# Performance work log

Hardware: AMD Instinct MI355X
Metric: run time of the kernel (lower is better)

## Reference

```python
import jax, jax.numpy as jnp
import numpy as np

N_NODES = 50000
N_EDGES = 800000
NUM_FEATURES = 128
HIDDEN = 128
NUM_CLASSES = 32


def gcn_conv(x, src, dst, n, W, b):
    loop = jnp.arange(n)
    s = jnp.concatenate([src, loop])
    d = jnp.concatenate([dst, loop])
    deg = jax.ops.segment_sum(jnp.ones_like(d, dtype=x.dtype), d, num_segments=n)
    dinv = jnp.where(deg > 0, jax.lax.rsqrt(deg), 0.0)
    norm = dinv[s] * dinv[d]                      # [E+n]
    h = x @ W                                     # [n, out]
    msg = h[s] * norm[:, None]                    # gather + scale
    out = jax.ops.segment_sum(msg, d, num_segments=n)  # scatter-add
    return out + b


def setup_inputs() -> dict:
    key = jax.random.key(0)
    ks = jax.random.split(key, 9)
    x = jax.random.normal(ks[0], (N_NODES, NUM_FEATURES), dtype=jnp.float32)
    edge_index = jax.random.randint(ks[1], (2, N_EDGES), 0, N_NODES, dtype=jnp.int64)
    sc1 = 1.0 / np.sqrt(NUM_FEATURES)
    sc2 = 1.0 / np.sqrt(HIDDEN)
    W1 = jax.random.uniform(ks[2], (NUM_FEATURES, HIDDEN), jnp.float32, -sc1, sc1)
    b1 = jnp.zeros((HIDDEN,), jnp.float32)
    W2 = jax.random.uniform(ks[3], (HIDDEN, HIDDEN), jnp.float32, -sc2, sc2)
    b2 = jnp.zeros((HIDDEN,), jnp.float32)
    Wfc = jax.random.uniform(ks[4], (HIDDEN, NUM_CLASSES), jnp.float32, -sc2, sc2)
    bfc = jax.random.uniform(ks[5], (NUM_CLASSES,), jnp.float32, -sc2, sc2)
    return {"x": x, "edge_index": edge_index, "W1": W1, "b1": b1,
            "W2": W2, "b2": b2, "Wfc": Wfc, "bfc": bfc}


def reference(x, edge_index, W1, b1, W2, b2, Wfc, bfc):
    n = x.shape[0]
    src, dst = edge_index[0], edge_index[1]
    h = jax.nn.relu(gcn_conv(x, src, dst, n, W1, b1))
    h = jax.nn.relu(gcn_conv(h, src, dst, n, W2, b2))
    # global_mean_pool with batch = zeros -> mean over all nodes, shape [1, HIDDEN]
    pooled = jnp.mean(h, axis=0, keepdims=True)
    return pooled @ Wfc + bfc  # [1, NUM_CLASSES]
```

## Files before the change

kernel.cpp:

```cpp
#include <hip/hip_runtime.h>
#include <stdint.h>

#define FEAT 128
#define ECH 2048
#define CAP 200000

typedef short bf16x8 __attribute__((ext_vector_type(8)));
typedef float f32x4 __attribute__((ext_vector_type(4)));
typedef float f32x2 __attribute__((ext_vector_type(2)));

__device__ __forceinline__ float bfs(unsigned short u) {
    uint32_t t = ((uint32_t)u) << 16;
    return __builtin_bit_cast(float, t);
}
__device__ __forceinline__ unsigned short f2bf(float f) {
    uint32_t u = __builtin_bit_cast(uint32_t, f);
    u += 0x7fffu + ((u >> 16) & 1u);
    return (unsigned short)(u >> 16);
}

__launch_bounds__(256)
__global__ void k_prep(const int* __restrict__ ei,
                       int* __restrict__ dstb, int* __restrict__ srcb,
                       int* __restrict__ bcnt, int* __restrict__ deg,
                       int E, int n, int psz, int NE,
                       const void* W1, const void* W2,
                       const void* b1, const void* b2,
                       const void* Wfc, const void* bfc,
                       unsigned short* Wth1, unsigned short* Wth2,
                       float* b1f, float* b2f, float* Wfcf, float* bfcf) {
    int t = threadIdx.x;

    if ((int)blockIdx.x >= NE) {
        __shared__ int hits;
        int blk = blockIdx.x - NE;
        const void* sampsrc = (blk < 32) ? W1 : (blk < 64 ? W2 : Wfc);
        const uint32_t* samp = (const uint32_t*)sampsrc;
        if (t == 0) hits = 0;
        __syncthreads();
        unsigned ew = (samp[t] >> 7) & 0xFFu;
        unsigned long long bl = __ballot(ew >= 0x60u && ew <= 0x90u);
        if ((t & 63) == 0) atomicAdd(&hits, (int)__popcll(bl));
        __syncthreads();
        int isbf = (2 * hits > 256);

        if (blk < 64) {
            const void* W = (blk < 32) ? W1 : W2;
            unsigned short* th = (blk < 32) ? Wth1 : Wth2;
            int base = (blk & 31) * 512;
            #pragma unroll
            for (int j = 0; j < 2; j++) {
                int idx = base + t * 2 + j;
                int nn = idx >> 7, k = idx & 127;
                int si = k * 128 + nn;
                float f = isbf ? bfs(((const unsigned short*)W)[si])
                               : ((const float*)W)[si];
                th[nn * 128 + k] = f2bf(f);
            }
        } else {
            int i = (blk - 64) * 256 + t;
            if (i >= 4384) return;
            const void* src; float* dst; int off;
            if (i < 128)       { src = b1;  dst = b1f;  off = i; }
            else if (i < 256)  { src = b2;  dst = b2f;  off = i - 128; }
            else if (i < 4352) { src = Wfc; dst = Wfcf; off = i - 256; }
            else               { src = bfc; dst = bfcf; off = i - 4352; }
            dst[off] = isbf ? bfs(((const unsigned short*)src)[off])
                            : ((const float*)src)[off];
        }
        return;
    }

    __shared__ int lflag;
    __shared__ int cnt[8], lofs[8], gbase[8];
    __shared__ int stage_s[ECH];
    __shared__ int stage_d[ECH];
    __shared__ char sb[ECH];
    if (t < 128) {
        int di = blockIdx.x * 128 + t;
        if (di < n) deg[di] = 0;
    }
    if (t == 0) lflag = 0;
    if (t < 8) cnt[t] = 0;
    __syncthreads();
    if (ei[1 + 2 * t] != 0) atomicOr(&lflag, 1);
    __syncthreads();
    int is32 = lflag;

    int base = blockIdx.x * ECH;
    int s[8], d[8], p[8], slot[8];
    #pragma unroll
    for (int j = 0; j < 8; j++) {
        int e = base + j * 256 + t;
        int ss = 0, dd = 0;
        if (e < E) {
            ss = is32 ? ei[e]     : ei[2 * e];
            dd = is32 ? ei[E + e] : ei[2 * E + 2 * e];
            if ((unsigned)ss >= (unsigned)n) ss = 0;
            if ((unsigned)dd >= (unsigned)n) dd = 0;
            int pp = dd / psz;
            if (pp > 7) pp = 7;
            p[j] = pp;
            slot[j] = atomicAdd(&cnt[pp], 1);
        } else p[j] = -1;
        s[j] = ss; d[j] = dd;
    }
    __syncthreads();
    if (t == 0) {
        int acc = 0;
        #pragma unroll
        for (int i = 0; i < 8; i++) { lofs[i] = acc; acc += cnt[i]; }
    }
    __syncthreads();
    if (t < 8) gbase[t] = atomicAdd(&bcnt[t], cnt[t]);
    __syncthreads();
    #pragma unroll
    for (int j = 0; j < 8; j++) {
        if (p[j] >= 0) {
            int pos = lofs[p[j]] + slot[j];
            stage_s[pos] = s[j];
            stage_d[pos] = d[j];
            sb[pos] = (char)p[j];
        }
    }
    __syncthreads();
    int tot = lofs[7] + cnt[7];
    for (int i = t; i < tot; i += 256) {
        int pp = sb[i];
        int off = gbase[pp] + (i - lofs[pp]);
        if (off < CAP) {
            dstb[pp * CAP + off] = stage_d[i];
            srcb[pp * CAP + off] = stage_s[i];
        }
    }
}

__launch_bounds__(256)
__global__ void k_degp(const int* __restrict__ dstb, const int* __restrict__ bcnt,
                       int* __restrict__ deg) {
    int p = blockIdx.x & 7;
    int nb = gridDim.x >> 3;
    int cnt = bcnt[p]; if (cnt > CAP) cnt = CAP;
    const int* db = dstb + p * CAP;
    for (int i = (blockIdx.x >> 3) * 256 + threadIdx.x; i < cnt; i += nb * 256)
        atomicAdd(&deg[db[i]], 1);
}

__global__ void k_bsum(const int* __restrict__ deg, int* __restrict__ bsum,
                       float* __restrict__ dinv, int n) {
    __shared__ int ws[4];
    int t = threadIdx.x, lane = t & 63, w = t >> 6;
    int idx = blockIdx.x * 256 + t;
    int v = (idx < n) ? deg[idx] : 0;
    if (idx < n) dinv[idx] = rsqrtf((float)(v + 1));
    int r = v;
    #pragma unroll
    for (int off = 32; off > 0; off >>= 1) r += __shfl_down(r, off, 64);
    if (lane == 0) ws[w] = r;
    __syncthreads();
    if (t == 0) bsum[blockIdx.x] = ws[0] + ws[1] + ws[2] + ws[3];
}

__launch_bounds__(256)
__global__ void k_bapply2(const int* __restrict__ deg, const int* __restrict__ bsum,
                          int* __restrict__ row_ptr, int* __restrict__ cursor,
                          int n, int nb) {
    __shared__ int wred[4];
    __shared__ int wsum[4];
    __shared__ int boffs;
    int b = blockIdx.x, t = threadIdx.x, lane = t & 63, w = t >> 6;

    int pv = (t < b && t < nb) ? bsum[t] : 0;
    #pragma unroll
    for (int off = 32; off > 0; off >>= 1) pv += __shfl_down(pv, off, 64);
    if (lane == 0) wred[w] = pv;
    __syncthreads();
    if (t == 0) boffs = wred[0] + wred[1] + wred[2] + wred[3];
    __syncthreads();

    int idx = b * 256 + t;
    int v = (idx < n) ? deg[idx] : 0;
    int s = v;
    #pragma unroll
    for (int off = 1; off < 64; off <<= 1) {
        int x = __shfl_up(s, off, 64);
        if (lane >= off) s += x;
    }
    if (lane == 63) wsum[w] = s;
    __syncthreads();
    if (t == 0) {
        int acc = 0;
        #pragma unroll
        for (int i = 0; i < 4; i++) { int x = wsum[i]; wsum[i] = acc; acc += x; }
    }
    __syncthreads();
    int ex = boffs + s - v + wsum[w];
    if (idx < n) {
        row_ptr[idx] = ex;
        cursor[idx]  = ex;
    }
    if (idx == n - 1) row_ptr[n] = ex + v;
}

__launch_bounds__(256)
__global__ void k_scatp(const int* __restrict__ dstb, const int* __restrict__ srcb,
                        const int* __restrict__ bcnt,
                        int* __restrict__ cursor, int* __restrict__ col, int E) {
    int p = blockIdx.x & 7;
    int nb = gridDim.x >> 3;
    int cnt = bcnt[p]; if (cnt > CAP) cnt = CAP;
    const int* db = dstb + p * CAP;
    const int* sb = srcb + p * CAP;
    for (int i = (blockIdx.x >> 3) * 256 + threadIdx.x; i < cnt; i += nb * 256) {
        int pos = atomicAdd(&cursor[db[i]], 1);
        if ((unsigned)pos < (unsigned)E) col[pos] = sb[i];
    }
}

__launch_bounds__(256)
__global__ void k_gemm(const void* __restrict__ X,
                       const unsigned short* __restrict__ Wth,
                       const float* __restrict__ dinv,
                       uint32_t* __restrict__ hs8, int n, int fmt) {
    __shared__ unsigned char lds8[4][16 * 128];
    int wave = threadIdx.x >> 6;
    int l = threadIdx.x & 63;
    int quad = l >> 4;
    int m16 = l & 15;
    int r0 = (blockIdx.x * 4 + wave) * 16;

    int isbf;
    if (fmt != 0) isbf = 1;
    else {
        unsigned ew = (((const uint32_t*)X)[l] >> 7) & 0xFFu;
        unsigned long long bl = __ballot(ew >= 0x60u && ew <= 0x90u);
        isbf = ((int)__popcll(bl) * 2 > 64) ? 1 : 0;
    }

    int ra = r0 + m16;
    if (ra > n - 1) ra = n - 1;
    bf16x8 ah[4];
    if (fmt == 2) {
        const uint2* Xq = (const uint2*)X;
        #pragma unroll
        for (int kt = 0; kt < 4; kt++) {
            uint2 v8 = Xq[ra * 16 + kt * 4 + quad];
            f32x2 p0 = __builtin_amdgcn_cvt_pk_f32_fp8((int)v8.x, false);
            f32x2 p1 = __builtin_amdgcn_cvt_pk_f32_fp8((int)v8.x, true);
            f32x2 p2 = __builtin_amdgcn_cvt_pk_f32_fp8((int)v8.y, false);
            f32x2 p3 = __builtin_amdgcn_cvt_pk_f32_fp8((int)v8.y, true);
            bf16x8 h;
            h[0] = (short)f2bf(p0.x); h[1] = (short)f2bf(p0.y);
            h[2] = (short)f2bf(p1.x); h[3] = (short)f2bf(p1.y);
            h[4] = (short)f2bf(p2.x); h[5] = (short)f2bf(p2.y);
            h[6] = (short)f2bf(p3.x); h[7] = (short)f2bf(p3.y);
            ah[kt] = h;
        }
    } else if (isbf) {
        const int4* Xv = (const int4*)X;
        #pragma unroll
        for (int kt = 0; kt < 4; kt++)
            ah[kt] = __builtin_bit_cast(bf16x8, Xv[ra * 16 + kt * 4 + quad]);
    } else {
        const float4* Xf = (const float4*)X;
        #pragma unroll
        for (int kt = 0; kt < 4; kt++) {
            int jj = kt * 4 + quad;
            float4 fa = Xf[ra * 32 + jj * 2];
            float4 fb = Xf[ra * 32 + jj * 2 + 1];
            float v[8] = {fa.x, fa.y, fa.z, fa.w, fb.x, fb.y, fb.z, fb.w};
            bf16x8 h;
            #pragma unroll
            for (int j = 0; j < 8; j++) h[j] = (short)f2bf(v[j]);
            ah[kt] = h;
        }
    }

    float dv[4];
    #pragma unroll
    for (int reg = 0; reg < 4; reg++) {
        int row = r0 + quad * 4 + reg;
        if (row > n - 1) row = n - 1;
        dv[reg] = dinv[row];
    }

    const int4* Wvh = (const int4*)Wth;
    #pragma unroll
    for (int nt = 0; nt < 8; nt++) {
        f32x4 acc = {0.f, 0.f, 0.f, 0.f};
        int brow = (nt * 16 + m16) * 16;
        #pragma unroll
        for (int kt = 0; kt < 4; kt++) {
            bf16x8 bh = __builtin_bit_cast(bf16x8, Wvh[brow + kt * 4 + quad]);
            acc = __builtin_amdgcn_mfma_f32_16x16x32_bf16(ah[kt], bh, acc, 0, 0, 0);
        }
        #pragma unroll
        for (int reg = 0; reg < 4; reg++) {
            float v = acc[reg] * dv[reg];
            int pk = __builtin_amdgcn_cvt_pk_fp8_f32(v, v, 0, false);
            lds8[wave][(quad * 4 + reg) * 128 + nt * 16 + m16] = (unsigned char)(pk & 0xFF);
        }
    }
    __syncthreads();
    const uint32_t* l32 = (const uint32_t*)lds8[wave];
    #pragma unroll
    for (int i = 0; i < 8; i++) {
        int idx = i * 64 + l;
        int row = idx >> 5;
        int grow = r0 + row;
        if (grow < n) hs8[grow * 32 + (idx & 31)] = l32[idx];
    }
}

__launch_bounds__(256)
__global__ void k_agg(const unsigned short* __restrict__ hsv,
                      const int* __restrict__ row_ptr,
                      const int* __restrict__ col, const float* __restrict__ dinv,
                      const float* __restrict__ bias,
                      unsigned short* __restrict__ out8, float* __restrict__ partial,
                      int n, int E) {
    __shared__ float pl[4][128];
    int wave = threadIdx.x >> 6;
    int lane = threadIdx.x & 63;
    int node = blockIdx.x * 4 + wave;
    bool active = (node < n);
    int nd = active ? node : 0;

    f32x2 sf = __builtin_amdgcn_cvt_pk_f32_fp8((int)hsv[nd * 64 + lane], false);
    float a0 = sf.x, a1 = sf.y;

    int e = row_ptr[nd];
    int end = active ? row_ptr[nd + 1] : e;
    if (e < 0) e = 0;
    if (end > E) end = E;

    for (; e + 16 <= end; e += 16) {
        unsigned si[16];
        #pragma unroll
        for (int j = 0; j < 16; j++) {
            unsigned s = (unsigned)col[e + j];
            si[j] = (s < (unsigned)n) ? s : 0u;
        }
        int uu[16];
        #pragma unroll
        for (int j = 0; j < 16; j++) uu[j] = hsv[si[j] * 64 + lane];
        #pragma unroll
        for (int j = 0; j < 16; j++) {
            f32x2 f = __builtin_amdgcn_cvt_pk_f32_fp8(uu[j], false);
            a0 += f.x;
            a1 += f.y;
        }
    }
    for (; e + 8 <= end; e += 8) {
        unsigned si[8];
        #pragma unroll
        for (int j = 0; j < 8; j++) {
            unsigned s = (unsigned)col[e + j];
            si[j] = (s < (unsigned)n) ? s : 0u;
        }
        int uu[8];
        #pragma unroll
        for (int j = 0; j < 8; j++) uu[j] = hsv[si[j] * 64 + lane];
        #pragma unroll
        for (int j = 0; j < 8; j++) {
            f32x2 f = __builtin_amdgcn_cvt_pk_f32_fp8(uu[j], false);
            a0 += f.x;
            a1 += f.y;
        }
    }
    for (; e < end; ++e) {
        unsigned s0 = (unsigned)col[e];
        if (s0 >= (unsigned)n) s0 = 0;
        f32x2 f = __builtin_amdgcn_cvt_pk_f32_fp8((int)hsv[s0 * 64 + lane], false);
        a0 += f.x;
        a1 += f.y;
    }

    float dv = dinv[nd];
    float2 bu = ((const float2*)bias)[lane];
    float r0 = fmaxf(dv * a0 + bu.x, 0.f);
    float r1 = fmaxf(dv * a1 + bu.y, 0.f);
    if (!active) { r0 = 0.f; r1 = 0.f; }

    if (out8 != nullptr && active) {
        int pk = __builtin_amdgcn_cvt_pk_fp8_f32(r0, r1, 0, false);
        out8[node * 64 + lane] = (unsigned short)(pk & 0xFFFF);
    }
    if (partial != nullptr) {
        pl[wave][2 * lane]     = r0;
        pl[wave][2 * lane + 1] = r1;
        __syncthreads();
        int t = threadIdx.x;
        if (t < 128) {
            float ps = pl[0][t] + pl[1][t] + pl[2][t] + pl[3][t];
            partial[blockIdx.x * 128 + t] = ps;
        }
    }
}

__launch_bounds__(256)
__global__ void k_redfinal(const float* __restrict__ partial, float* __restrict__ pooled,
                           int* __restrict__ done,
                           const float* __restrict__ Wfcf, const float* __restrict__ bfcf,
                           const void* __restrict__ x, void* __restrict__ out,
                           int n, int nbrows, int gblocks) {
    __shared__ float red[8][128];
    int t = threadIdx.x;
    int chunk = (nbrows + gblocks - 1) / gblocks;
    int r0 = blockIdx.x * chunk;
    int r1 = r0 + chunk;
    if (r1 > nbrows) r1 = nbrows;

    float4 acc = {0.f, 0.f, 0.f, 0.f};
    const float4* p4 = (const float4*)partial;
    for (int i = r0 * 32 + t; i < r1 * 32; i += 256) {
        float4 v = p4[i];
        acc.x += v.x; acc.y += v.y; acc.z += v.z; acc.w += v.w;
    }
    int g = t >> 5;
    int fb = (t & 31) * 4;
    red[g][fb]     = acc.x;
    red[g][fb + 1] = acc.y;
    red[g][fb + 2] = acc.z;
    red[g][fb + 3] = acc.w;
    __syncthreads();
    if (t < 128) {
        float s = red[0][t] + red[1][t] + red[2][t] + red[3][t]
                + red[4][t] + red[5][t] + red[6][t] + red[7][t];
        atomicAdd(&pooled[t], s);
    }
    __threadfence();
    __shared__ int lastf;
    if (t == 0) lastf = (atomicAdd(done, 1) == gblocks - 1) ? 1 : 0;
    __syncthreads();
    if (!lastf) return;

    __shared__ int hits;
    __shared__ float pv[128];
    if (t == 0) hits = 0;
    __syncthreads();
    unsigned ew = (((const uint32_t*)x)[t] >> 7) & 0xFFu;
    unsigned long long bl = __ballot(ew >= 0x60u && ew <= 0x90u);
    if ((t & 63) == 0) atomicAdd(&hits, (int)__popcll(bl));
    if (t < 128)
        pv[t] = __hip_atomic_load(&pooled[t], __ATOMIC_RELAXED,
                                  __HIP_MEMORY_SCOPE_AGENT);
    __syncthreads();
    int isbf = (2 * hits > 256);
    if (t < 32) {
        float s = 0.f;
        for (int c = 0; c < 128; ++c) s += pv[c] * Wfcf[c * 32 + t];
        s = s * (1.0f / (float)n) + bfcf[t];
        if (isbf) ((unsigned short*)out)[t] = f2bf(s);
        else      ((float*)out)[t] = s;
    }
}


extern "C" void kernel_launch(void* const* d_in, const int* in_sizes, int n_in,
                              void* d_out, int out_size, void* d_ws, size_t ws_size,
                              hipStream_t stream) {
    const void* x   = d_in[0];
    const int*  ei  = (const int*)d_in[1];
    const void* W1  = d_in[2];
    const void* b1  = d_in[3];
    const void* W2  = d_in[4];
    const void* b2  = d_in[5];
    const void* Wfc = d_in[6];
    const void* bfc = d_in[7];

    const int n = in_sizes[0] / FEAT;
    const int E = in_sizes[1] / 2;
    const int nagg = (n + 3) / 4;
    const int psz  = (n + 7) / 8;
    const int nscan = (n + 255) / 256;
    const int NE   = (E + ECH - 1) / ECH;

    char* ws = (char*)d_ws;
    uint32_t*       hs8     = (uint32_t*)(ws);
    unsigned short* act8    = (unsigned short*)(ws + 12800000);
    float*          partial = (float*)(ws + 25600000);
    int*            col     = (int*)(ws + 38400000);
    int*            dstb    = (int*)(ws + 41600000);
    int*            srcb    = (int*)(ws + 48000000);
    int*            deg     = (int*)(ws + 54400000);
    int*            row_ptr = (int*)(ws + 54600000);
    int*            cursor  = (int*)(ws + 54800016);
    float*          dinv    = (float*)(ws + 55000016);
    unsigned short* Wth1    = (unsigned short*)(ws + 55200016);
    unsigned short* Wth2    = (unsigned short*)(ws + 55232784);
    float*          b1f     = (float*)(ws + 55265552);
    float*          b2f     = (float*)(ws + 55266064);
    float*          Wfcf    = (float*)(ws + 55266576);
    float*          bfcf    = (float*)(ws + 55282960);
    float*          pooled  = (float*)(ws + 55283088);
    int*            bcnt    = (int*)(ws + 55283600);
    int*            done    = (int*)(ws + 55283632);
    int*            bsum    = (int*)(ws + 55283648);

    if (ws_size < 55284448) return;

    hipMemsetAsync(pooled, 0, 1344, stream);

    k_prep<<<NE + 82, 256, 0, stream>>>(ei, dstb, srcb, bcnt, deg, E, n, psz, NE,
                                        W1, W2, b1, b2, Wfc, bfc,
                                        Wth1, Wth2, b1f, b2f, Wfcf, bfcf);
    k_degp<<<512, 256, 0, stream>>>(dstb, bcnt, deg);
    k_bsum<<<nscan, 256, 0, stream>>>(deg, bsum, dinv, n);
    k_bapply2<<<nscan, 256, 0, stream>>>(deg, bsum, row_ptr, cursor, n, nscan);
    k_scatp<<<512, 256, 0, stream>>>(dstb, srcb, bcnt, cursor, col, E);

    int gemm_grid = (n + 63) / 64;
    k_gemm<<<gemm_grid, 256, 0, stream>>>(x, Wth1, dinv, hs8, n, 0);
    k_agg<<<nagg, 256, 0, stream>>>((const unsigned short*)hs8, row_ptr, col, dinv,
                                    b1f, act8, nullptr, n, E);
    k_gemm<<<gemm_grid, 256, 0, stream>>>(act8, Wth2, dinv, hs8, n, 2);
    k_agg<<<nagg, 256, 0, stream>>>((const unsigned short*)hs8, row_ptr, col, dinv,
                                    b2f, nullptr, partial, n, E);
    k_redfinal<<<100, 256, 0, stream>>>(partial, pooled, done, Wfcf, bfcf,
                                        x, d_out, n, nagg, 100);
}
```

Before: 297.1 us.

## Fuse CSR scatter with first GEMM and layer-1 aggregation with second GEMM

The CSR column scatter and the first-layer GEMM now run as disjoint block ranges of a single launch, since they do not depend on each other. The first-layer aggregation is fused with the second-layer GEMM: each block aggregates 16 nodes into LDS as bf16 and immediately multiplies by W2, so the fp8 activation buffer is never written to or read back from global memory. This removes two launches and one global round-trip, and keeps the layer-1 activations in bf16 rather than fp8. In exchange, each wave now aggregates 4 nodes serially, and the 16-wide gather unroll is dropped from the aggregation loops, which may reduce memory-level parallelism.

```diff
diff --git a/kernel.cpp b/kernel.cpp
--- a/kernel.cpp
+++ b/kernel.cpp
@@ -4,6 +4,7 @@
 #define FEAT 128
 #define ECH 2048
 #define CAP 200000
+#define SCB 512
 
 typedef short bf16x8 __attribute__((ext_vector_type(8)));
 typedef float f32x4 __attribute__((ext_vector_type(4)));
@@ -202,61 +203,24 @@
     if (idx == n - 1) row_ptr[n] = ex + v;
 }
 
-__launch_bounds__(256)
-__global__ void k_scatp(const int* __restrict__ dstb, const int* __restrict__ srcb,
-                        const int* __restrict__ bcnt,
-                        int* __restrict__ cursor, int* __restrict__ col, int E) {
-    int p = blockIdx.x & 7;
-    int nb = gridDim.x >> 3;
-    int cnt = bcnt[p]; if (cnt > CAP) cnt = CAP;
-    const int* db = dstb + p * CAP;
-    const int* sb = srcb + p * CAP;
-    for (int i = (blockIdx.x >> 3) * 256 + threadIdx.x; i < cnt; i += nb * 256) {
-        int pos = atomicAdd(&cursor[db[i]], 1);
-        if ((unsigned)pos < (unsigned)E) col[pos] = sb[i];
-    }
-}
-
-__launch_bounds__(256)
-__global__ void k_gemm(const void* __restrict__ X,
-                       const unsigned short* __restrict__ Wth,
-                       const float* __restrict__ dinv,
-                       uint32_t* __restrict__ hs8, int n, int fmt) {
-    __shared__ unsigned char lds8[4][16 * 128];
-    int wave = threadIdx.x >> 6;
-    int l = threadIdx.x & 63;
+__device__ __forceinline__ void gemm_body(const void* __restrict__ X,
+                                          const unsigned short* __restrict__ Wth,
+                                          const float* __restrict__ dinv,
+                                          uint32_t* __restrict__ hs8,
+                                          int n, int tile, int l,
+                                          unsigned char* __restrict__ ldsrow) {
     int quad = l >> 4;
     int m16 = l & 15;
-    int r0 = (blockIdx.x * 4 + wave) * 16;
-
-    int isbf;
-    if (fmt != 0) isbf = 1;
-    else {
-        unsigned ew = (((const uint32_t*)X)[l] >> 7) & 0xFFu;
-        unsigned long long bl = __ballot(ew >= 0x60u && ew <= 0x90u);
-        isbf = ((int)__popcll(bl) * 2 > 64) ? 1 : 0;
-    }
+    int r0 = tile * 16;
+
+    unsigned ew = (((const uint32_t*)X)[l] >> 7) & 0xFFu;
+    unsigned long long bl = __ballot(ew >= 0x60u && ew <= 0x90u);
+    int isbf = ((int)__popcll(bl) * 2 > 64) ? 1 : 0;
 
     int ra = r0 + m16;
     if (ra > n - 1) ra = n - 1;
     bf16x8 ah[4];
-    if (fmt == 2) {
-        const uint2* Xq = (const uint2*)X;
-        #pragma unroll
-        for (int kt = 0; kt < 4; kt++) {
-            uint2 v8 = Xq[ra * 16 + kt * 4 + quad];
-            f32x2 p0 = __builtin_amdgcn_cvt_pk_f32_fp8((int)v8.x, false);
-            f32x2 p1 = __builtin_amdgcn_cvt_pk_f32_fp8((int)v8.x, true);
-            f32x2 p2 = __builtin_amdgcn_cvt_pk_f32_fp8((int)v8.y, false);
-            f32x2 p3 = __builtin_amdgcn_cvt_pk_f32_fp8((int)v8.y, true);
-            bf16x8 h;
-            h[0] = (short)f2bf(p0.x); h[1] = (short)f2bf(p0.y);
-            h[2] = (short)f2bf(p1.x); h[3] = (short)f2bf(p1.y);
-            h[4] = (short)f2bf(p2.x); h[5] = (short)f2bf(p2.y);
-            h[6] = (short)f2bf(p3.x); h[7] = (short)f2bf(p3.y);
-            ah[kt] = h;
-        }
-    } else if (isbf) {
+    if (isbf) {
         const int4* Xv = (const int4*)X;
         #pragma unroll
         for (int kt = 0; kt < 4; kt++)
@@ -298,11 +262,11 @@
         for (int reg = 0; reg < 4; reg++) {
             float v = acc[reg] * dv[reg];
             int pk = __builtin_amdgcn_cvt_pk_fp8_f32(v, v, 0, false);
-            lds8[wave][(quad * 4 + reg) * 128 + nt * 16 + m16] = (unsigned char)(pk & 0xFF);
-        }
-    }
-    __syncthreads();
-    const uint32_t* l32 = (const uint32_t*)lds8[wave];
+            ldsrow[(quad * 4 + reg) * 128 + nt * 16 + m16] = (unsigned char)(pk & 0xFF);
+        }
+    }
+    __syncthreads();
+    const uint32_t* l32 = (const uint32_t*)ldsrow;
     #pragma unroll
     for (int i = 0; i < 8; i++) {
         int idx = i * 64 + l;
@@ -313,12 +277,145 @@
 }
 
 __launch_bounds__(256)
+__global__ void k_sg(const int* __restrict__ dstb, const int* __restrict__ srcb,
+                     const int* __restrict__ bcnt,
+                     int* __restrict__ cursor, int* __restrict__ col, int E,
+                     const void* __restrict__ X,
+                     const unsigned short* __restrict__ Wth,
+                     const float* __restrict__ dinv,
+                     uint32_t* __restrict__ hs8, int n) {
+    __shared__ unsigned char lds8[4][16 * 128];
+    int b = blockIdx.x;
+    if (b < SCB) {
+        int p = b & 7;
+        int nb = SCB >> 3;
+        int cnt = bcnt[p]; if (cnt > CAP) cnt = CAP;
+        const int* db = dstb + p * CAP;
+        const int* sb = srcb + p * CAP;
+        for (int i = (b >> 3) * 256 + threadIdx.x; i < cnt; i += nb * 256) {
+            int pos = atomicAdd(&cursor[db[i]], 1);
+            if ((unsigned)pos < (unsigned)E) col[pos] = sb[i];
+        }
+        return;
+    }
+    int wave = threadIdx.x >> 6;
+    int l = threadIdx.x & 63;
+    gemm_body(X, Wth, dinv, hs8, n, (b - SCB) * 4 + wave, l, lds8[wave]);
+}
+
+__launch_bounds__(256)
+__global__ void k_agg1gemm2(const unsigned short* __restrict__ hsv,
+                            const int* __restrict__ row_ptr,
+                            const int* __restrict__ col,
+                            const float* __restrict__ dinv,
+                            const float* __restrict__ bias,
+                            const unsigned short* __restrict__ Wth2,
+                            uint32_t* __restrict__ hs8out, int n, int E) {
+    __shared__ unsigned short actlds[16 * 136];
+    __shared__ unsigned char pack[16 * 128];
+    int wave = threadIdx.x >> 6;
+    int lane = threadIdx.x & 63;
+    int tile0 = blockIdx.x * 16;
+
+    for (int i = 0; i < 4; i++) {
+        int node = tile0 + wave * 4 + i;
+        bool active = (node < n);
+        int nd = active ? node : 0;
+
+        f32x2 sf = __builtin_amdgcn_cvt_pk_f32_fp8((int)hsv[nd * 64 + lane], false);
+        float a0 = sf.x, a1 = sf.y;
+
+        int e = row_ptr[nd];
+        int end = active ? row_ptr[nd + 1] : e;
+        if (e < 0) e = 0;
+        if (end > E) end = E;
+
+        for (; e + 8 <= end; e += 8) {
+            unsigned si[8];
+            #pragma unroll
+            for (int j = 0; j < 8; j++) {
+                unsigned s = (unsigned)col[e + j];
+                si[j] = (s < (unsigned)n) ? s : 0u;
+            }
+            int uu[8];
+            #pragma unroll
+            for (int j = 0; j < 8; j++) uu[j] = hsv[si[j] * 64 + lane];
+            #pragma unroll
+            for (int j = 0; j < 8; j++) {
+                f32x2 f = __builtin_amdgcn_cvt_pk_f32_fp8(uu[j], false);
+                a0 += f.x;
+                a1 += f.y;
+            }
+        }
+        for (; e < end; ++e) {
+            unsigned s0 = (unsigned)col[e];
+            if (s0 >= (unsigned)n) s0 = 0;
+            f32x2 f = __builtin_amdgcn_cvt_pk_f32_fp8((int)hsv[s0 * 64 + lane], false);
+            a0 += f.x;
+            a1 += f.y;
+        }
+
+        float dv = dinv[nd];
+        float2 bu = ((const float2*)bias)[lane];
+        float r0 = fmaxf(dv * a0 + bu.x, 0.f);
+        float r1 = fmaxf(dv * a1 + bu.y, 0.f);
+        if (!active) { r0 = 0.f; r1 = 0.f; }
+        int row = wave * 4 + i;
+        actlds[row * 136 + 2 * lane]     = f2bf(r0);
+        actlds[row * 136 + 2 * lane + 1] = f2bf(r1);
+    }
+    __syncthreads();
+
+    int quad = lane >> 4;
+    int m16 = lane & 15;
+    bf16x8 ah[4];
+    #pragma unroll
+    for (int kt = 0; kt < 4; kt++) {
+        const unsigned short* p = &actlds[m16 * 136 + kt * 32 + quad * 8];
+        ah[kt] = __builtin_bit_cast(bf16x8, *(const int4*)p);
+    }
+    float dv4[4];
+    #pragma unroll
+    for (int reg = 0; reg < 4; reg++) {
+        int row = tile0 + quad * 4 + reg;
+        if (row > n - 1) row = n - 1;
+        dv4[reg] = dinv[row];
+    }
+    const int4* Wvh = (const int4*)Wth2;
+    #pragma unroll
+    for (int ntl = 0; ntl < 2; ntl++) {
+        int nt = wave * 2 + ntl;
+        f32x4 acc = {0.f, 0.f, 0.f, 0.f};
+        int brow = (nt * 16 + m16) * 16;
+        #pragma unroll
+        for (int kt = 0; kt < 4; kt++) {
+            bf16x8 bh = __builtin_bit_cast(bf16x8, Wvh[brow + kt * 4 + quad]);
+            acc = __builtin_amdgcn_mfma_f32_16x16x32_bf16(ah[kt], bh, acc, 0, 0, 0);
+        }
+        #pragma unroll
+        for (int reg = 0; reg < 4; reg++) {
+            float v = acc[reg] * dv4[reg];
+            int pk = __builtin_amdgcn_cvt_pk_fp8_f32(v, v, 0, false);
+            pack[(quad * 4 + reg) * 128 + nt * 16 + m16] = (unsigned char)(pk & 0xFF);
+        }
+    }
+    __syncthreads();
+    const uint32_t* l32 = (const uint32_t*)pack;
+    #pragma unroll
+    for (int i = 0; i < 2; i++) {
+        int idx = i * 256 + threadIdx.x;
+        int row = idx >> 5;
+        int grow = tile0 + row;
+        if (grow < n) hs8out[grow * 32 + (idx & 31)] = l32[idx];
+    }
+}
+
+__launch_bounds__(256)
 __global__ void k_agg(const unsigned short* __restrict__ hsv,
                       const int* __restrict__ row_ptr,
                       const int* __restrict__ col, const float* __restrict__ dinv,
                       const float* __restrict__ bias,
-                      unsigned short* __restrict__ out8, float* __restrict__ partial,
-                      int n, int E) {
+                      float* __restrict__ partial, int n, int E) {
     __shared__ float pl[4][128];
     int wave = threadIdx.x >> 6;
     int lane = threadIdx.x & 63;
@@ -334,23 +431,6 @@
     if (e < 0) e = 0;
     if (end > E) end = E;
 
-    for (; e + 16 <= end; e += 16) {
-        unsigned si[16];
-        #pragma unroll
-        for (int j = 0; j < 16; j++) {
-            unsigned s = (unsigned)col[e + j];
-            si[j] = (s < (unsigned)n) ? s : 0u;
-        }
-        int uu[16];
-        #pragma unroll
-        for (int j = 0; j < 16; j++) uu[j] = hsv[si[j] * 64 + lane];
-        #pragma unroll
-        for (int j = 0; j < 16; j++) {
-            f32x2 f = __builtin_amdgcn_cvt_pk_f32_fp8(uu[j], false);
-            a0 += f.x;
-            a1 += f.y;
-        }
-    }
     for (; e + 8 <= end; e += 8) {
         unsigned si[8];
         #pragma unroll
@@ -382,19 +462,13 @@
     float r1 = fmaxf(dv * a1 + bu.y, 0.f);
     if (!active) { r0 = 0.f; r1 = 0.f; }
 
-    if (out8 != nullptr && active) {
-        int pk = __builtin_amdgcn_cvt_pk_fp8_f32(r0, r1, 0, false);
-        out8[node * 64 + lane] = (unsigned short)(pk & 0xFFFF);
-    }
-    if (partial != nullptr) {
-        pl[wave][2 * lane]     = r0;
-        pl[wave][2 * lane + 1] = r1;
-        __syncthreads();
-        int t = threadIdx.x;
-        if (t < 128) {
-            float ps = pl[0][t] + pl[1][t] + pl[2][t] + pl[3][t];
-            partial[blockIdx.x * 128 + t] = ps;
-        }
+    pl[wave][2 * lane]     = r0;
+    pl[wave][2 * lane + 1] = r1;
+    __syncthreads();
+    int t = threadIdx.x;
+    if (t < 128) {
+        float ps = pl[0][t] + pl[1][t] + pl[2][t] + pl[3][t];
+        partial[blockIdx.x * 128 + t] = ps;
     }
 }
 
@@ -472,13 +546,15 @@
     const int n = in_sizes[0] / FEAT;
     const int E = in_sizes[1] / 2;
     const int nagg = (n + 3) / 4;
+    const int ntile = (n + 15) / 16;
     const int psz  = (n + 7) / 8;
     const int nscan = (n + 255) / 256;
     const int NE   = (E + ECH - 1) / ECH;
+    const int gemm_grid = (ntile + 3) / 4;
 
     char* ws = (char*)d_ws;
     uint32_t*       hs8     = (uint32_t*)(ws);
-    unsigned short* act8    = (unsigned short*)(ws + 12800000);
+    uint32_t*       hs8b    = (uint32_t*)(ws + 12800000);
     float*          partial = (float*)(ws + 25600000);
     int*            col     = (int*)(ws + 38400000);
     int*            dstb    = (int*)(ws + 41600000);
@@ -508,15 +584,12 @@
     k_degp<<<512, 256, 0, stream>>>(dstb, bcnt, deg);
     k_bsum<<<nscan, 256, 0, stream>>>(deg, bsum, dinv, n);
     k_bapply2<<<nscan, 256, 0, stream>>>(deg, bsum, row_ptr, cursor, n, nscan);
-    k_scatp<<<512, 256, 0, stream>>>(dstb, srcb, bcnt, cursor, col, E);
-
-    int gemm_grid = (n + 63) / 64;
-    k_gemm<<<gemm_grid, 256, 0, stream>>>(x, Wth1, dinv, hs8, n, 0);
-    k_agg<<<nagg, 256, 0, stream>>>((const unsigned short*)hs8, row_ptr, col, dinv,
-                                    b1f, act8, nullptr, n, E);
-    k_gemm<<<gemm_grid, 256, 0, stream>>>(act8, Wth2, dinv, hs8, n, 2);
-    k_agg<<<nagg, 256, 0, stream>>>((const unsigned short*)hs8, row_ptr, col, dinv,
-                                    b2f, nullptr, partial, n, E);
+    k_sg<<<SCB + gemm_grid, 256, 0, stream>>>(dstb, srcb, bcnt, cursor, col, E,
+                                              x, Wth1, dinv, hs8, n);
+    k_agg1gemm2<<<ntile, 256, 0, stream>>>((const unsigned short*)hs8, row_ptr,
+                                           col, dinv, b1f, Wth2, hs8b, n, E);
+    k_agg<<<nagg, 256, 0, stream>>>((const unsigned short*)hs8b, row_ptr, col,
+                                    dinv, b2f, partial, n, E);
     k_redfinal<<<100, 256, 0, stream>>>(partial, pooled, done, Wfcf, bfcf,
                                         x, d_out, n, nagg, 100);
 }
```

Measured after the change: 277.4 us. 1.07x faster.
